# Performance work log

Measured on AMD Instinct MI355X. Metric: run time of the kernel, lower is better.

Reference implementation:

```python
import jax, jax.numpy as jnp
import numpy as np

D = 256      # wsi_projection_dim / SNN hidden
E = 1024     # wsi_embedding_dim
N = 60000    # num WSI patches
H = 8        # n_heads
DH = D // H  # head dim
K = 3        # int(6 * topk_ratio)
SIZES = (100, 200, 300, 400, 500, 600)
NC = 4       # num_classes
EPS = 1e-5


def _ln(x, g, b):
    m = x.mean(-1, keepdims=True)
    v = ((x - m) ** 2).mean(-1, keepdims=True)
    return (x - m) / jnp.sqrt(v + EPS) * g + b


def setup_inputs() -> dict:
    key = jax.random.key(0)
    ks = iter(jax.random.split(key, 64))
    sc = 0.02
    inp = {}
    inp["x_path"] = jax.random.normal(next(ks), (1, N, E), dtype=jnp.float32)
    for i, s in enumerate(SIZES):
        inp[f"x_omic{i+1}"] = jax.random.normal(next(ks), (s,), dtype=jnp.float32)
    # per-pathway SNN blocks: Linear(size,256)+ELU, Linear(256,256)+ELU
    for i, s in enumerate(SIZES):
        inp[f"sw1_{i}"] = sc * jax.random.normal(next(ks), (s, D), dtype=jnp.float32)
    inp["sb1"] = jnp.zeros((len(SIZES), D), jnp.float32)
    inp["sw2"] = sc * jax.random.normal(next(ks), (len(SIZES), D, D), dtype=jnp.float32)
    inp["sb2"] = jnp.zeros((len(SIZES), D), jnp.float32)
    # wsi projection
    inp["wp"] = sc * jax.random.normal(next(ks), (E, D), dtype=jnp.float32)
    inp["bp"] = jnp.zeros((D,), jnp.float32)
    # gene attention MLP 256->64->1
    inp["wa1"] = sc * jax.random.normal(next(ks), (D, 64), dtype=jnp.float32)
    inp["ba1"] = jnp.zeros((64,), jnp.float32)
    inp["wa2"] = sc * jax.random.normal(next(ks), (64, 1), dtype=jnp.float32)
    inp["ba2"] = jnp.zeros((1,), jnp.float32)
    # MultiheadAttention projections
    for nm in ("wq", "wk", "wv", "wo"):
        inp[nm] = sc * jax.random.normal(next(ks), (D, D), dtype=jnp.float32)
    for nm in ("bq", "bk", "bv", "bo"):
        inp[nm] = jnp.zeros((D,), jnp.float32)
    inp["ln1_g"] = jnp.ones((D,), jnp.float32)
    inp["ln1_b"] = jnp.zeros((D,), jnp.float32)
    # bilinear fusion 512->256->256
    inp["wf1"] = sc * jax.random.normal(next(ks), (2 * D, D), dtype=jnp.float32)
    inp["bf1"] = jnp.zeros((D,), jnp.float32)
    inp["wf2"] = sc * jax.random.normal(next(ks), (D, D), dtype=jnp.float32)
    inp["bf2"] = jnp.zeros((D,), jnp.float32)
    inp["ln2_g"] = jnp.ones((D,), jnp.float32)
    inp["ln2_b"] = jnp.zeros((D,), jnp.float32)
    inp["wc"] = sc * jax.random.normal(next(ks), (D, NC), dtype=jnp.float32)
    inp["bc"] = jnp.zeros((NC,), jnp.float32)
    return inp


def _forward(x_path, x_omics, sw1s, sb1, sw2, sb2, wp, bp, wa1, ba1, wa2, ba2,
             wq, bq, wk, bk, wv, bv, wo, bo, ln1_g, ln1_b,
             wf1, bf1, wf2, bf2, ln2_g, ln2_b, wc, bc):
    # per-pathway SNN (eval: AlphaDropout = identity)
    h = [jax.nn.elu(jax.nn.elu(x @ w1 + sb1[i]) @ sw2[i] + sb2[i])
         for i, (x, w1) in enumerate(zip(x_omics, sw1s))]
    bag = jnp.stack(h)[None]                      # [1, G, D]
    # gene selection: softmax -> topk -> gather (mask*gather == gather)
    scores = (jax.nn.relu(bag @ wa1 + ba1) @ wa2 + ba2)[..., 0]   # [1, G]
    attw = jax.nn.softmax(scores, axis=1)
    _, idx = jax.lax.top_k(attw, K)               # [1, K]
    selected = jnp.take_along_axis(bag, idx[..., None], axis=1)  # [1, K, D]
    # wsi projection (eval: Dropout = identity)
    wsi = jax.nn.relu(x_path @ wp + bp)           # [1, N, D]
    # cross-attention: queries = selected genes, keys/values = wsi patches
    q = (selected @ wq + bq).reshape(1, K, H, DH).transpose(0, 2, 1, 3)
    k_ = (wsi @ wk + bk).reshape(1, N, H, DH).transpose(0, 2, 1, 3)
    v_ = (wsi @ wv + bv).reshape(1, N, H, DH).transpose(0, 2, 1, 3)
    att = jax.nn.softmax(jnp.einsum('bhqd,bhkd->bhqk', q, k_) / np.float32(np.sqrt(DH)), axis=-1)
    attn_out = jnp.einsum('bhqk,bhkd->bhqd', att, v_).transpose(0, 2, 1, 3).reshape(1, K, D)
    attn_out = attn_out @ wo + bo                 # [1, K, D]
    # adaptive_avg_pool2d over N -> K bins (N divisible by K -> equal bins)
    pooled = wsi.reshape(1, K, N // K, D).mean(axis=2)  # [1, K, D]
    attended = _ln(attn_out + pooled, ln1_g, ln1_b)
    attended_mean = attended.mean(axis=1)         # [1, D]
    gene_features = selected.mean(axis=1)         # [1, D]
    comb = jnp.concatenate([attended_mean, gene_features], axis=1)  # [1, 2D]
    f = jax.nn.relu(comb @ wf1 + bf1)
    f = jax.nn.relu(f @ wf2 + bf2)
    fused = _ln(f + attended_mean, ln2_g, ln2_b)
    return fused @ wc + bc                        # [1, num_classes]


def reference(x_path, x_omic1, x_omic2, x_omic3, x_omic4, x_omic5, x_omic6,
              sw1_0, sw1_1, sw1_2, sw1_3, sw1_4, sw1_5, sb1, sw2, sb2,
              wp, bp, wa1, ba1, wa2, ba2,
              wq, bq, wk, bk, wv, bv, wo, bo, ln1_g, ln1_b,
              wf1, bf1, wf2, bf2, ln2_g, ln2_b, wc, bc):
    x_omics = (x_omic1, x_omic2, x_omic3, x_omic4, x_omic5, x_omic6)
    sw1s = (sw1_0, sw1_1, sw1_2, sw1_3, sw1_4, sw1_5)
    return _forward(x_path, x_omics, sw1s, sb1, sw2, sb2, wp, bp, wa1, ba1, wa2, ba2,
                    wq, bq, wk, bk, wv, bv, wo, bo, ln1_g, ln1_b,
                    wf1, bf1, wf2, bf2, ln2_g, ln2_b, wc, bc)
```

## Files before the change

### kernel.cpp

```cpp
#include <hip/hip_runtime.h>
#include <hip/hip_bf16.h>
#include <math.h>

typedef unsigned short ushort_t;
typedef __attribute__((ext_vector_type(8))) short bf16x8;
typedef __attribute__((ext_vector_type(4))) float f32x4;

#define NHQ 24
#define LN_EPS 1e-5f
#define NBLK_F 469
#define NBLK_A 938
#define NPOOL 256

#define WS_BAG 0
#define WS_SEL 1536
#define WS_GENE 2304
#define WS_PM 3584
#define WS_PL 28160
#define WS_PACC 52736
#define WS_PPOOL 839168
#define WS_ATTN 1232384
#define WS_POOLED 1233152
#define WS_BF16 1233920
#define U_WPT 0
#define U_WKT 262144
#define U_WVT 327680
#define U_QB  393216
#define U_WSIP 401408
#define WS_SPLIT_BYTES 36474880ULL

__device__ __forceinline__ ushort_t f2bf(float f) {
    __hip_bfloat16 h = __float2bfloat16(f);
    return *reinterpret_cast<ushort_t*>(&h);
}
__device__ __forceinline__ float bf2f(unsigned int u) {
    union { unsigned int i; float f; } c; c.i = u << 16; return c.f;
}
__device__ __forceinline__ unsigned int pk2(float a, float b) {
    return (unsigned int)f2bf(a) | ((unsigned int)f2bf(b) << 16);
}

__global__ void prep_kernel(const float* __restrict__ wp, const float* __restrict__ wk,
                            const float* __restrict__ wv, ushort_t* __restrict__ ub) {
    const int b = blockIdx.x, t = threadIdx.x;
    if (b < 16) {
        const int D16 = b;
        for (int i = 0; i < 64; ++i) {
            int f = t + i * 256;
            int K32 = f >> 9, r = f & 511;
            int lg = r >> 7, lm2 = (r >> 3) & 15, e = r & 7;
            int k = K32 * 32 + lg * 8 + e, d = D16 * 16 + lm2;
            ub[U_WPT + D16 * 16384 + f] = f2bf(wp[(size_t)k * 256 + d]);
        }
    } else if (b < 32) {
        const int D16 = b - 16;
        for (int i = 0; i < 16; ++i) {
            int f = t + i * 256;
            int K32 = f >> 9, r = f & 511;
            int lg = r >> 7, lm2 = (r >> 3) & 15, e = r & 7;
            int k = K32 * 32 + lg * 8 + e, d = D16 * 16 + lm2;
            ub[U_WKT + D16 * 4096 + f] = f2bf(wk[(size_t)k * 256 + d]);
        }
    } else {
        const int D16 = b - 32;
        for (int i = 0; i < 16; ++i) {
            int f = t + i * 256;
            int K32 = f >> 9, r = f & 511;
            int lg = r >> 7, lm2 = (r >> 3) & 15, e = r & 7;
            int k = K32 * 32 + lg * 8 + e, d = D16 * 16 + lm2;
            ub[U_WVT + D16 * 4096 + f] = f2bf(wv[(size_t)k * 256 + d]);
        }
    }
}

struct PrepArgs {
    const float* xo[6];
    const float* w1[6];
    int sz[6];
};

__global__ void snn_kernel(PrepArgs pa, const float* __restrict__ sb1,
                           const float* __restrict__ sw2, const float* __restrict__ sb2,
                           float* __restrict__ bag) {
    __shared__ float xsh[600];
    __shared__ float t1sh[256];
    const int i = blockIdx.x;
    const int t = threadIdx.x;
    const int s = pa.sz[i];
    const float* xo = pa.xo[i];
    const float* w1 = pa.w1[i];
    for (int j = t; j < s; j += 256) xsh[j] = xo[j];
    __syncthreads();
    float acc = sb1[i * 256 + t];
    for (int j = 0; j < s; ++j) acc += xsh[j] * w1[j * 256 + t];
    t1sh[t] = acc > 0.f ? acc : expm1f(acc);
    __syncthreads();
    float acc2 = sb2[i * 256 + t];
    const float* w2 = sw2 + (size_t)i * 256 * 256;
    for (int j = 0; j < 256; ++j) acc2 += t1sh[j] * w2[j * 256 + t];
    bag[i * 256 + t] = acc2 > 0.f ? acc2 : expm1f(acc2);
}

__global__ void select_kernel(const float* __restrict__ wa1, const float* __restrict__ ba1,
                              const float* __restrict__ wa2, const float* __restrict__ ba2,
                              const float* __restrict__ wq, const float* __restrict__ bq,
                              float* __restrict__ wsf, ushort_t* __restrict__ ub) {
    __shared__ float bsh[6][256];
    __shared__ float ysh[64];
    __shared__ float ssh[8];
    __shared__ int isel[3];
    const int t = threadIdx.x;
    for (int j = t; j < 1536; j += 256) ((float*)bsh)[j] = wsf[WS_BAG + j];
    __syncthreads();
    for (int i = 0; i < 6; ++i) {
        if (t < 64) {
            float acc = ba1[t];
            for (int j = 0; j < 256; ++j) acc += bsh[i][j] * wa1[j * 64 + t];
            ysh[t] = fmaxf(acc, 0.f) * wa2[t];
        }
        __syncthreads();
        if (t == 0) {
            float sc = ba2[0];
            for (int j = 0; j < 64; ++j) sc += ysh[j];
            ssh[i] = sc;
        }
        __syncthreads();
    }
    if (t == 0) {
        float sc[6];
        for (int i = 0; i < 6; ++i) sc[i] = ssh[i];
        for (int k = 0; k < 3; ++k) {
            int best = 0; float bv = sc[0];
            for (int i = 1; i < 6; ++i) if (sc[i] > bv) { bv = sc[i]; best = i; }
            isel[k] = best;
            sc[best] = -INFINITY;
        }
    }
    __syncthreads();
    float g = 0.f;
    for (int k = 0; k < 3; ++k) {
        float v = bsh[isel[k]][t];
        wsf[WS_SEL + k * 256 + t] = v;
        g += v;
    }
    wsf[WS_GENE + t] = g * (1.f / 3.f);
    for (int kq = 0; kq < 3; ++kq) {
        float acc = bq[t];
        const float* srow = bsh[isel[kq]];
        for (int j = 0; j < 256; ++j) acc += srow[j] * wq[j * 256 + t];
        float v = acc * 0.17677669529663687f;
        int hq = (t >> 5) * 3 + kq, dd = t & 31;
        ub[U_QB + hq * 32 + dd] = f2bf(v);
    }
}


#define PLOAD_X(xr, c) { \
    _Pragma("unroll") for (int i_ = 0; i_ < 4; ++i_) { \
        int f_ = tid + i_ * 512; int p_ = f_ >> 4, c4_ = f_ & 15; \
        if (n0 + p_ < 60000) \
            xr[i_] = *(const float4*)(xp + (size_t)(n0 + p_) * 1024 + (c) * 64 + c4_ * 4); \
        else { xr[i_].x = 0.f; xr[i_].y = 0.f; xr[i_].z = 0.f; xr[i_].w = 0.f; } } }

#define PSTORE_X(xr, buf) { \
    _Pragma("unroll") for (int i_ = 0; i_ < 4; ++i_) { \
        int f_ = tid + i_ * 512; int p_ = f_ >> 4, c4_ = f_ & 15; \
        int byte_ = (p_ * 128 + c4_ * 8) ^ ((p_ & 7) << 4); \
        uint2 u_; u_.x = pk2(xr[i_].x, xr[i_].y); u_.y = pk2(xr[i_].z, xr[i_].w); \
        *(uint2*)((buf) + byte_) = u_; } }

__global__ __launch_bounds__(512, 4) void proj_kernel(
    const float* __restrict__ xp, const float* __restrict__ bp,
    const ushort_t* __restrict__ ub, ushort_t* __restrict__ wsiP)
{
    __shared__ __align__(16) char xbuf[2][16384];
    const int tid = threadIdx.x;
    const int b = blockIdx.x;
    const int lane = tid & 63;
    const int w = tid >> 6;
    const int lm = lane & 15;
    const int lg = lane >> 4;
    const int wd0 = (w & 3) * 64;
    const int n0 = b * 128;
    const ushort_t* wpP = ub + U_WPT;

    f32x4 acc[16];
#pragma unroll
    for (int i = 0; i < 16; ++i) acc[i] = (f32x4){0.f, 0.f, 0.f, 0.f};

    float4 xr[4];
    PLOAD_X(xr, 0);
    PSTORE_X(xr, xbuf[0]);
    PLOAD_X(xr, 1);
    __syncthreads();
#pragma unroll 1
    for (int c = 0; c < 16; ++c) {
        const char* cur = xbuf[c & 1];
        if (c < 15) PSTORE_X(xr, xbuf[(c + 1) & 1]);
        if (c < 14) PLOAD_X(xr, c + 2);
#pragma unroll
        for (int ks = 0; ks < 2; ++ks) {
            bf16x8 wf[4];
#pragma unroll
            for (int dt = 0; dt < 4; ++dt)
                wf[dt] = *(const bf16x8*)(wpP + ((size_t)(((w & 3) * 4 + dt) * 32 + c * 2 + ks)) * 512 + lane * 8);
            bf16x8 bfr[4];
#pragma unroll
            for (int pt = 0; pt < 4; ++pt) {
                int p = (w >> 2) * 64 + pt * 16 + lm;
                int byte = (p * 128 + ks * 64 + lg * 16) ^ ((p & 7) << 4);
                bfr[pt] = *(const bf16x8*)(cur + byte);
            }
#pragma unroll
            for (int dt = 0; dt < 4; ++dt)
#pragma unroll
                for (int pt = 0; pt < 4; ++pt)
                    acc[dt * 4 + pt] = __builtin_amdgcn_mfma_f32_16x16x32_bf16(wf[dt], bfr[pt], acc[dt * 4 + pt], 0, 0, 0);
        }
        __syncthreads();
    }
#pragma unroll
    for (int dt = 0; dt < 4; ++dt) {
        int d0 = wd0 + dt * 16 + lg * 4;
        float4 bb = *(const float4*)(bp + d0);
        int ks2 = d0 >> 5, lg2 = (d0 >> 3) & 3, e0 = d0 & 7;
#pragma unroll
        for (int pt = 0; pt < 4; ++pt) {
            int p16 = b * 8 + (w >> 2) * 4 + pt;
            f32x4 v = acc[dt * 4 + pt];
            uint2 u;
            u.x = pk2(fmaxf(v[0] + bb.x, 0.f), fmaxf(v[1] + bb.y, 0.f));
            u.y = pk2(fmaxf(v[2] + bb.z, 0.f), fmaxf(v[3] + bb.w, 0.f));
            *(uint2*)(wsiP + (size_t)((p16 * 8 + ks2) * 4 + lg2) * 128 + lm * 8 + e0) = u;
        }
    }
}

__global__ __launch_bounds__(256, 4) void attn_kernel(
    const float* __restrict__ bk, const float* __restrict__ bv,
    const ushort_t* __restrict__ ub, const ushort_t* __restrict__ wsiP,
    float* __restrict__ wsf)
{
    __shared__ __align__(16) ushort_t kv_s[64 * 256];
    __shared__ __align__(16) ushort_t p_s[24 * 64];
    const int tid = threadIdx.x;
    const int b = blockIdx.x;
    const int lane = tid & 63, w = tid >> 6;
    const int lm = lane & 15, lg = lane >> 4;
    const int lmc = lm < 3 ? lm : 2;
    const int n0 = b * 64;
    const int wd0 = w * 64;
    const ushort_t* wkP = ub + U_WKT;
    const ushort_t* wvP = ub + U_WVT;

    {
        f32x4 acc[16];
#pragma unroll
        for (int i = 0; i < 16; ++i) acc[i] = (f32x4){0.f, 0.f, 0.f, 0.f};
#pragma unroll
        for (int ks = 0; ks < 8; ++ks) {
            bf16x8 wf[4], bfr[4];
#pragma unroll
            for (int dt = 0; dt < 4; ++dt)
                wf[dt] = *(const bf16x8*)(wkP + ((size_t)((w * 4 + dt) * 8 + ks)) * 512 + lane * 8);
#pragma unroll
            for (int pt = 0; pt < 4; ++pt)
                bfr[pt] = *(const bf16x8*)(wsiP + (size_t)(((b * 4 + pt) * 8 + ks) * 4 + lg) * 128 + lm * 8);
#pragma unroll
            for (int dt = 0; dt < 4; ++dt)
#pragma unroll
                for (int pt = 0; pt < 4; ++pt)
                    acc[dt * 4 + pt] = __builtin_amdgcn_mfma_f32_16x16x32_bf16(wf[dt], bfr[pt], acc[dt * 4 + pt], 0, 0, 0);
        }
#pragma unroll
        for (int dt = 0; dt < 4; ++dt) {
            int d0 = wd0 + dt * 16 + lg * 4;
            float4 bb = *(const float4*)(bk + d0);
#pragma unroll
            for (int pt = 0; pt < 4; ++pt) {
                int p = pt * 16 + lm;
                f32x4 v = acc[dt * 4 + pt];
                uint2 u;
                u.x = pk2(v[0] + bb.x, v[1] + bb.y);
                u.y = pk2(v[2] + bb.z, v[3] + bb.w);
                int byte = (p * 512 + d0 * 2) ^ ((p & 7) << 4);
                *(uint2*)((char*)kv_s + byte) = u;
            }
        }
    }
    __syncthreads();

    float m_reg[2], l_reg[2];
#pragma unroll
    for (int hh = 0; hh < 2; ++hh) {
        int h = w * 2 + hh;
        bf16x8 qf;
        if (lm < 3) qf = *(const bf16x8*)(ub + U_QB + (h * 3 + lm) * 32 + lg * 8);
        else { bf16x8 z = {0,0,0,0,0,0,0,0}; qf = z; }
        f32x4 sc[4];
#pragma unroll
        for (int blk = 0; blk < 4; ++blk) {
            sc[blk] = (f32x4){0.f, 0.f, 0.f, 0.f};
            int p = blk * 16 + lm;
            int byte = (p * 512 + (h * 32 + lg * 8) * 2) ^ ((p & 7) << 4);
            bf16x8 kf = *(const bf16x8*)((const char*)kv_s + byte);
            sc[blk] = __builtin_amdgcn_mfma_f32_16x16x32_bf16(kf, qf, sc[blk], 0, 0, 0);
        }
        float tmax = -INFINITY;
#pragma unroll
        for (int blk = 0; blk < 4; ++blk)
#pragma unroll
            for (int j = 0; j < 4; ++j) {
                int p = blk * 16 + lg * 4 + j;
                if (n0 + p >= 60000) sc[blk][j] = -INFINITY;
                tmax = fmaxf(tmax, sc[blk][j]);
            }
        tmax = fmaxf(tmax, __shfl_xor(tmax, 16));
        tmax = fmaxf(tmax, __shfl_xor(tmax, 32));
        float lsum = 0.f;
#pragma unroll
        for (int blk = 0; blk < 4; ++blk)
#pragma unroll
            for (int j = 0; j < 4; ++j) {
                float e = __expf(sc[blk][j] - tmax);
                sc[blk][j] = e;
                lsum += e;
            }
        lsum += __shfl_xor(lsum, 16);
        lsum += __shfl_xor(lsum, 32);
        m_reg[hh] = tmax;
        l_reg[hh] = lsum;
        if (lm < 3) {
#pragma unroll
            for (int blk = 0; blk < 4; ++blk) {
                int p0 = blk * 16 + lg * 4;
                *(unsigned int*)(p_s + (h * 3 + lm) * 64 + p0) = pk2(sc[blk][0], sc[blk][1]);
                *(unsigned int*)(p_s + (h * 3 + lm) * 64 + p0 + 2) = pk2(sc[blk][2], sc[blk][3]);
            }
        }
    }
    __syncthreads();

    {
        f32x4 acc[16];
#pragma unroll
        for (int i = 0; i < 16; ++i) acc[i] = (f32x4){0.f, 0.f, 0.f, 0.f};
#pragma unroll
        for (int ks = 0; ks < 8; ++ks) {
            bf16x8 wf[4], bfr[4];
#pragma unroll
            for (int dt = 0; dt < 4; ++dt)
                wf[dt] = *(const bf16x8*)(wvP + ((size_t)((w * 4 + dt) * 8 + ks)) * 512 + lane * 8);
#pragma unroll
            for (int pt = 0; pt < 4; ++pt)
                bfr[pt] = *(const bf16x8*)(wsiP + (size_t)(((b * 4 + pt) * 8 + ks) * 4 + lg) * 128 + lm * 8);
#pragma unroll
            for (int dt = 0; dt < 4; ++dt)
#pragma unroll
                for (int pt = 0; pt < 4; ++pt)
                    acc[dt * 4 + pt] = __builtin_amdgcn_mfma_f32_16x16x32_bf16(wf[dt], bfr[pt], acc[dt * 4 + pt], 0, 0, 0);
        }
        __syncthreads();
#pragma unroll
        for (int dt = 0; dt < 4; ++dt) {
            int d0 = wd0 + dt * 16 + lg * 4;
            float4 bb = *(const float4*)(bv + d0);
#pragma unroll
            for (int pt = 0; pt < 4; ++pt) {
                int p = pt * 16 + lm;
                f32x4 v = acc[dt * 4 + pt];
                float r[4] = {v[0] + bb.x, v[1] + bb.y, v[2] + bb.z, v[3] + bb.w};
#pragma unroll
                for (int j = 0; j < 4; ++j) {
                    int dd = d0 + j;
                    int byte = (dd * 128 + p * 2) ^ ((dd & 7) << 4);
                    *(ushort_t*)((char*)kv_s + byte) = f2bf(r[j]);
                }
            }
        }
    }
    __syncthreads();

    f32x4 pv[2][2];
#pragma unroll
    for (int hh = 0; hh < 2; ++hh)
#pragma unroll
        for (int nb = 0; nb < 2; ++nb) pv[hh][nb] = (f32x4){0.f, 0.f, 0.f, 0.f};
#pragma unroll
    for (int hh = 0; hh < 2; ++hh) {
        int h = w * 2 + hh;
#pragma unroll
        for (int ks = 0; ks < 2; ++ks) {
            bf16x8 pa = *(const bf16x8*)(p_s + (h * 3 + lmc) * 64 + ks * 32 + lg * 8);
#pragma unroll
            for (int nb = 0; nb < 2; ++nb) {
                int row = h * 32 + nb * 16 + lm;
                int byte = (row * 128 + (ks * 32 + lg * 8) * 2) ^ ((row & 7) << 4);
                bf16x8 vb = *(const bf16x8*)((const char*)kv_s + byte);
                pv[hh][nb] = __builtin_amdgcn_mfma_f32_16x16x32_bf16(pa, vb, pv[hh][nb], 0, 0, 0);
            }
        }
    }

    if (lg == 0) {
#pragma unroll
        for (int hh = 0; hh < 2; ++hh)
#pragma unroll
            for (int nb = 0; nb < 2; ++nb)
#pragma unroll
                for (int j = 0; j < 3; ++j) {
                    int hq = (w * 2 + hh) * 3 + j;
                    wsf[WS_PACC + b * 768 + hq * 32 + nb * 16 + lm] = pv[hh][nb][j];
                }
    }
    if (lm < 3 && lg == 0) {
#pragma unroll
        for (int hh = 0; hh < 2; ++hh) {
            int hq = (w * 2 + hh) * 3 + lm;
            wsf[WS_PM + b * 24 + hq] = m_reg[hh];
            wsf[WS_PL + b * 24 + hq] = l_reg[hh];
        }
    }
}

__global__ __launch_bounds__(256, 8) void pool_kernel(const ushort_t* __restrict__ wsiP,
                                                      float* __restrict__ wsf) {
    const int tid = threadIdx.x, b = blockIdx.x;
    const int lane = tid & 63;
    const int lm = lane & 15, lg = (lane >> 4) & 3;
    const int ks = ((b * 4) + (tid >> 6)) & 7;
    f32x4 s[3][2];
#pragma unroll
    for (int i = 0; i < 3; ++i) { s[i][0] = (f32x4){0,0,0,0}; s[i][1] = (f32x4){0,0,0,0}; }
    for (int sl = b * 256 + tid; sl < 1921024; sl += 65536) {
        int p16 = sl >> 9;
        if (p16 >= 3750) continue;
        uint4 u = *(const uint4*)(wsiP + (size_t)sl * 8);
        int bin = (p16 >= 2500) ? 2 : (p16 >= 1250 ? 1 : 0);
        f32x4 a, c;
        a[0] = bf2f(u.x & 0xffffu); a[1] = bf2f(u.x >> 16);
        a[2] = bf2f(u.y & 0xffffu); a[3] = bf2f(u.y >> 16);
        c[0] = bf2f(u.z & 0xffffu); c[1] = bf2f(u.z >> 16);
        c[2] = bf2f(u.w & 0xffffu); c[3] = bf2f(u.w >> 16);
        s[bin][0] += a; s[bin][1] += c;
    }
#pragma unroll
    for (int o = 1; o < 16; o <<= 1)
#pragma unroll
        for (int bin = 0; bin < 3; ++bin)
#pragma unroll
            for (int hv = 0; hv < 2; ++hv)
#pragma unroll
                for (int e = 0; e < 4; ++e)
                    s[bin][hv][e] += __shfl_xor(s[bin][hv][e], o);
    if (lm == 0) {
        int dbase = ks * 32 + lg * 8;
#pragma unroll
        for (int bin = 0; bin < 3; ++bin)
#pragma unroll
            for (int hv = 0; hv < 2; ++hv)
#pragma unroll
                for (int e = 0; e < 4; ++e)
                    wsf[WS_PPOOL + b * 768 + bin * 256 + dbase + hv * 4 + e] = s[bin][hv][e];
    } else if (lm == 1) {
        int dbase = (ks ^ 4) * 32 + lg * 8;
#pragma unroll
        for (int bin = 0; bin < 3; ++bin)
#pragma unroll
            for (int e = 0; e < 8; ++e)
                wsf[WS_PPOOL + b * 768 + bin * 256 + dbase + e] = 0.f;
    }
}

#define LOAD_X(xr, c) { \
    _Pragma("unroll") for (int i_ = 0; i_ < 4; ++i_) { \
        int f_ = tid + i_ * 512; int p_ = f_ >> 4, c4_ = f_ & 15; \
        if (n0 + p_ < 60000) \
            xr[i_] = *(const float4*)(xp + (size_t)(n0 + p_) * 1024 + (c) * 64 + c4_ * 4); \
        else { xr[i_].x = 0.f; xr[i_].y = 0.f; xr[i_].z = 0.f; xr[i_].w = 0.f; } } }

#define STORE_X(xr) { \
    _Pragma("unroll") for (int i_ = 0; i_ < 4; ++i_) { \
        int f_ = tid + i_ * 512; int p_ = f_ >> 4, c4_ = f_ & 15; \
        int byte_ = (p_ * 128 + c4_ * 8) ^ ((p_ & 7) << 4); \
        uint2 u_; u_.x = pk2(xr[i_].x, xr[i_].y); u_.y = pk2(xr[i_].z, xr[i_].w); \
        *(uint2*)((char*)x_s + byte_) = u_; } }

#define LOAD_W1(dst, c) { \
    _Pragma("unroll") for (int ks_ = 0; ks_ < 2; ++ks_) \
    _Pragma("unroll") for (int dt_ = 0; dt_ < 4; ++dt_) \
        dst[ks_ * 4 + dt_] = *(const bf16x8*)(wpP + ((size_t)(((w & 3) * 4 + dt_) * 32 + (c) * 2 + ks_)) * 512 + lane * 8); }

#define MFMA_CHUNK(wf) { \
    _Pragma("unroll") for (int ks_ = 0; ks_ < 2; ++ks_) { \
        bf16x8 bfr_[4]; \
        _Pragma("unroll") for (int pt_ = 0; pt_ < 4; ++pt_) { \
            int p_ = wp0 + pt_ * 16 + lm; \
            int byte_ = (p_ * 128 + ks_ * 64 + lg * 16) ^ ((p_ & 7) << 4); \
            bfr_[pt_] = *(const bf16x8*)((const char*)x_s + byte_); } \
        _Pragma("unroll") for (int dt_ = 0; dt_ < 4; ++dt_) \
        _Pragma("unroll") for (int pt_ = 0; pt_ < 4; ++pt_) \
            acc[dt_ * 4 + pt_] = __builtin_amdgcn_mfma_f32_16x16x32_bf16(wf[ks_ * 4 + dt_], bfr_[pt_], acc[dt_ * 4 + pt_], 0, 0, 0); } }

__global__ __launch_bounds__(512, 2) void main_kernel(
    const float* __restrict__ xp, const float* __restrict__ bp,
    const float* __restrict__ bk, const float* __restrict__ bv,
    const ushort_t* __restrict__ ub, float* __restrict__ wsf)
{
    __shared__ __align__(16) ushort_t wsi_s[128 * 256];
    __shared__ __align__(16) ushort_t kv_s[128 * 256];
    __shared__ __align__(16) ushort_t x_s[128 * 64];
    __shared__ __align__(16) ushort_t p_s[NHQ * 128];
    __shared__ float mlc_s[72];

    const int tid = threadIdx.x;
    const int b = blockIdx.x;
    const int lane = tid & 63;
    const int w = tid >> 6;
    const int lm = lane & 15;
    const int lg = lane >> 4;
    const int lmc = (lm < 3) ? lm : 2;
    const int wd0 = (w & 3) * 64;
    const int wp0 = (w >> 2) * 64;

    const ushort_t* wpP = ub + U_WPT;
    const ushort_t* wkP = ub + U_WKT;
    const ushort_t* wvP = ub + U_WVT;

    bf16x8 qfrag;
    if (lm < 3) qfrag = *(const bf16x8*)(ub + U_QB + (w * 3 + lm) * 32 + lg * 8);
    else { bf16x8 z = {0,0,0,0,0,0,0,0}; qfrag = z; }

    if (tid < 24) { mlc_s[tid] = -INFINITY; mlc_s[24 + tid] = 0.f; mlc_s[48 + tid] = 0.f; }

    f32x4 pv[2] = {{0.f,0.f,0.f,0.f},{0.f,0.f,0.f,0.f}};
    float pl0 = 0.f, pl1 = 0.f, pl2 = 0.f;
    __syncthreads();

    const int n0 = b * 128;
    {
        f32x4 acc[16];
#pragma unroll
        for (int i = 0; i < 16; ++i) acc[i] = (f32x4){0.f,0.f,0.f,0.f};
        float4 xr[4];
        bf16x8 wA[8], wB[8];
        LOAD_X(xr, 0); LOAD_W1(wA, 0);
        for (int c = 0; c < 16; c += 2) {
            __syncthreads();
            STORE_X(xr);
            __syncthreads();
            LOAD_X(xr, c + 1); LOAD_W1(wB, c + 1);
            MFMA_CHUNK(wA);
            __syncthreads();
            STORE_X(xr);
            __syncthreads();
            if (c + 2 < 16) { LOAD_X(xr, c + 2); LOAD_W1(wA, c + 2); }
            MFMA_CHUNK(wB);
        }
#pragma unroll
        for (int dt = 0; dt < 4; ++dt) {
            int d0 = wd0 + dt * 16 + lg * 4;
            float4 bb = *(const float4*)(bp + d0);
#pragma unroll
            for (int pt = 0; pt < 4; ++pt) {
                int p = wp0 + pt * 16 + lm;
                f32x4 v = acc[dt * 4 + pt];
                uint2 u;
                u.x = pk2(fmaxf(v[0] + bb.x, 0.f), fmaxf(v[1] + bb.y, 0.f));
                u.y = pk2(fmaxf(v[2] + bb.z, 0.f), fmaxf(v[3] + bb.w, 0.f));
                int byte = (p * 512 + d0 * 2) ^ ((p & 7) << 4);
                *(uint2*)((char*)wsi_s + byte) = u;
            }
        }
    }
    __syncthreads();

    {
        int d = tid & 255, half = tid >> 8;
#pragma unroll 16
        for (int pp = 0; pp < 64; ++pp) {
            int p = half * 64 + pp;
            int gp = n0 + p;
            int byte = (p * 512 + d * 2) ^ ((p & 7) << 4);
            float v = bf2f((unsigned int)*(const ushort_t*)((const char*)wsi_s + byte));
            pl0 += (gp < 20000) ? v : 0.f;
            pl1 += (gp >= 20000 && gp < 40000) ? v : 0.f;
            pl2 += (gp >= 40000 && gp < 60000) ? v : 0.f;
        }
    }

    {
        f32x4 acc2[16];
#pragma unroll
        for (int i = 0; i < 16; ++i) acc2[i] = (f32x4){0.f,0.f,0.f,0.f};
#pragma unroll
        for (int ks = 0; ks < 8; ++ks) {
            bf16x8 wf[4];
#pragma unroll
            for (int dt = 0; dt < 4; ++dt)
                wf[dt] = *(const bf16x8*)(wkP + ((size_t)(((w & 3) * 4 + dt) * 8 + ks)) * 512 + lane * 8);
            bf16x8 bfr[4];
#pragma unroll
            for (int pt = 0; pt < 4; ++pt) {
                int p = wp0 + pt * 16 + lm;
                int byte = (p * 512 + (ks * 32 + lg * 8) * 2) ^ ((p & 7) << 4);
                bfr[pt] = *(const bf16x8*)((const char*)wsi_s + byte);
            }
#pragma unroll
            for (int dt = 0; dt < 4; ++dt)
#pragma unroll
                for (int pt = 0; pt < 4; ++pt)
                    acc2[dt * 4 + pt] = __builtin_amdgcn_mfma_f32_16x16x32_bf16(wf[dt], bfr[pt], acc2[dt * 4 + pt], 0, 0, 0);
        }
#pragma unroll
        for (int dt = 0; dt < 4; ++dt) {
            int d0 = wd0 + dt * 16 + lg * 4;
            float4 bb = *(const float4*)(bk + d0);
#pragma unroll
            for (int pt = 0; pt < 4; ++pt) {
                int p = wp0 + pt * 16 + lm;
                f32x4 v = acc2[dt * 4 + pt];
                uint2 u;
                u.x = pk2(v[0] + bb.x, v[1] + bb.y);
                u.y = pk2(v[2] + bb.z, v[3] + bb.w);
                int byte = (p * 512 + d0 * 2) ^ ((p & 7) << 4);
                *(uint2*)((char*)kv_s + byte) = u;
            }
        }
    }
    __syncthreads();

    {
        f32x4 sc[8];
#pragma unroll
        for (int blk = 0; blk < 8; ++blk) {
            sc[blk] = (f32x4){0.f,0.f,0.f,0.f};
            int p = blk * 16 + lm;
            int byte = (p * 512 + (w * 32 + lg * 8) * 2) ^ ((p & 7) << 4);
            bf16x8 kf = *(const bf16x8*)((const char*)kv_s + byte);
            sc[blk] = __builtin_amdgcn_mfma_f32_16x16x32_bf16(kf, qfrag, sc[blk], 0, 0, 0);
        }
        float m_old = mlc_s[w * 3 + lmc];
        float tmax = -INFINITY;
#pragma unroll
        for (int blk = 0; blk < 8; ++blk)
#pragma unroll
            for (int j = 0; j < 4; ++j) {
                int p = blk * 16 + lg * 4 + j;
                if (n0 + p >= 60000) sc[blk][j] = -INFINITY;
                tmax = fmaxf(tmax, sc[blk][j]);
            }
        tmax = fmaxf(tmax, __shfl_xor(tmax, 16));
        tmax = fmaxf(tmax, __shfl_xor(tmax, 32));
        float mnew = fmaxf(m_old, tmax);
        float lsum = 0.f;
#pragma unroll
        for (int blk = 0; blk < 8; ++blk)
#pragma unroll
            for (int j = 0; j < 4; ++j) {
                float e = __expf(sc[blk][j] - mnew);
                sc[blk][j] = e;
                lsum += e;
            }
        lsum += __shfl_xor(lsum, 16);
        lsum += __shfl_xor(lsum, 32);
        float corr = __expf(m_old - mnew);
        if (lane < 3) {
            mlc_s[w * 3 + lane] = mnew;
            mlc_s[24 + w * 3 + lane] = mlc_s[24 + w * 3 + lane] * corr + lsum;
            mlc_s[48 + w * 3 + lane] = corr;
        }
        if (lm < 3) {
#pragma unroll
            for (int blk = 0; blk < 8; ++blk) {
                int p0 = blk * 16 + lg * 4;
                *(unsigned int*)(p_s + (w * 3 + lm) * 128 + p0) = pk2(sc[blk][0], sc[blk][1]);
                *(unsigned int*)(p_s + (w * 3 + lm) * 128 + p0 + 2) = pk2(sc[blk][2], sc[blk][3]);
            }
        }
    }
    __syncthreads();

    {
        f32x4 acc2[16];
#pragma unroll
        for (int i = 0; i < 16; ++i) acc2[i] = (f32x4){0.f,0.f,0.f,0.f};
#pragma unroll
        for (int ks = 0; ks < 8; ++ks) {
            bf16x8 wf[4];
#pragma unroll
            for (int dt = 0; dt < 4; ++dt)
                wf[dt] = *(const bf16x8*)(wvP + ((size_t)(((w & 3) * 4 + dt) * 8 + ks)) * 512 + lane * 8);
            bf16x8 bfr[4];
#pragma unroll
            for (int pt = 0; pt < 4; ++pt) {
                int p = wp0 + pt * 16 + lm;
                int byte = (p * 512 + (ks * 32 + lg * 8) * 2) ^ ((p & 7) << 4);
                bfr[pt] = *(const bf16x8*)((const char*)wsi_s + byte);
            }
#pragma unroll
            for (int dt = 0; dt < 4; ++dt)
#pragma unroll
                for (int pt = 0; pt < 4; ++pt)
                    acc2[dt * 4 + pt] = __builtin_amdgcn_mfma_f32_16x16x32_bf16(wf[dt], bfr[pt], acc2[dt * 4 + pt], 0, 0, 0);
        }
#pragma unroll
        for (int dt = 0; dt < 4; ++dt) {
            int d0 = wd0 + dt * 16 + lg * 4;
            float4 bb = *(const float4*)(bv + d0);
#pragma unroll
            for (int pt = 0; pt < 4; ++pt) {
                int p = wp0 + pt * 16 + lm;
                f32x4 v = acc2[dt * 4 + pt];
                float r[4] = {v[0] + bb.x, v[1] + bb.y, v[2] + bb.z, v[3] + bb.w};
#pragma unroll
                for (int j = 0; j < 4; ++j) {
                    int dd = d0 + j;
                    int byte = (dd * 256 + p * 2) ^ ((dd & 14) << 2);
                    *(ushort_t*)((char*)kv_s + byte) = f2bf(r[j]);
                }
            }
        }
    }
    __syncthreads();

    {
        float cj[4];
#pragma unroll
        for (int j = 0; j < 4; ++j) {
            int q = lg * 4 + j;
            cj[j] = mlc_s[48 + w * 3 + (q < 3 ? q : 2)];
        }
#pragma unroll
        for (int nb = 0; nb < 2; ++nb)
#pragma unroll
            for (int j = 0; j < 4; ++j) pv[nb][j] *= cj[j];
#pragma unroll
        for (int ks = 0; ks < 4; ++ks) {
            bf16x8 pa = *(const bf16x8*)(p_s + (w * 3 + lmc) * 128 + ks * 32 + lg * 8);
#pragma unroll
            for (int nb = 0; nb < 2; ++nb) {
                int row = w * 32 + nb * 16 + lm;
                int byte = (row * 256 + (ks * 32 + lg * 8) * 2) ^ ((row & 14) << 2);
                bf16x8 vb = *(const bf16x8*)((const char*)kv_s + byte);
                pv[nb] = __builtin_amdgcn_mfma_f32_16x16x32_bf16(pa, vb, pv[nb], 0, 0, 0);
            }
        }
    }

    __syncthreads();
    {
        float* scr = (float*)x_s;
        int d = tid & 255, half = tid >> 8;
        scr[half * 768 + 0 * 256 + d] = pl0;
        scr[half * 768 + 1 * 256 + d] = pl1;
        scr[half * 768 + 2 * 256 + d] = pl2;
    }
    __syncthreads();
    if (tid < 256) {
        float* scr = (float*)x_s;
#pragma unroll
        for (int bin = 0; bin < 3; ++bin)
            wsf[WS_PPOOL + b * 768 + bin * 256 + tid] = scr[bin * 256 + tid] + scr[768 + bin * 256 + tid];
    }
    if (tid < 24) {
        wsf[WS_PM + b * 24 + tid] = mlc_s[tid];
        wsf[WS_PL + b * 24 + tid] = mlc_s[24 + tid];
    }
    if (lg == 0) {
#pragma unroll
        for (int nb = 0; nb < 2; ++nb)
#pragma unroll
            for (int j = 0; j < 3; ++j) {
                int hq = w * 3 + j, dd = nb * 16 + lm;
                wsf[WS_PACC + b * 768 + hq * 32 + dd] = pv[nb][j];
            }
    }
}

__global__ __launch_bounds__(256) void combine_kernel(float* __restrict__ wsf, int nblk, int npool) {
    const int bidx = blockIdx.x;
    const int t = threadIdx.x;
    if (bidx < NHQ) {
        const int hq = bidx;
        __shared__ float w_s[1024];
        __shared__ float mred[4];
        __shared__ float lred[4];
        __shared__ float ored[8][32];
        float m = -INFINITY;
        for (int b = t; b < nblk; b += 256) m = fmaxf(m, wsf[WS_PM + b * 24 + hq]);
#pragma unroll
        for (int o = 32; o > 0; o >>= 1) m = fmaxf(m, __shfl_xor(m, o));
        if ((t & 63) == 0) mred[t >> 6] = m;
        __syncthreads();
        const float M = fmaxf(fmaxf(mred[0], mred[1]), fmaxf(mred[2], mred[3]));
        float L = 0.f;
        for (int b = t; b < nblk; b += 256) {
            float wv = __expf(wsf[WS_PM + b * 24 + hq] - M);
            w_s[b] = wv;
            L += wv * wsf[WS_PL + b * 24 + hq];
        }
#pragma unroll
        for (int o = 32; o > 0; o >>= 1) L += __shfl_xor(L, o);
        if ((t & 63) == 0) lred[t >> 6] = L;
        __syncthreads();
        const float Lt = lred[0] + lred[1] + lred[2] + lred[3];
        const int g = t >> 5, dd = t & 31;
        float O = 0.f;
        for (int b = g; b < nblk; b += 8)
            O += wsf[WS_PACC + b * 768 + hq * 32 + dd] * w_s[b];
        ored[g][dd] = O;
        __syncthreads();
        if (t < 32) {
            float s = 0.f;
#pragma unroll
            for (int g2 = 0; g2 < 8; ++g2) s += ored[g2][t];
            int h = hq / 3, kq = hq - h * 3;
            wsf[WS_ATTN + kq * 256 + h * 32 + t] = s / Lt;
        }
    } else {
        const int bin = bidx - NHQ;
        const int d = t;
        float s0 = 0.f, s1 = 0.f, s2 = 0.f, s3 = 0.f;
        int b = 0;
        for (; b + 3 < npool; b += 4) {
            s0 += wsf[WS_PPOOL + (b + 0) * 768 + bin * 256 + d];
            s1 += wsf[WS_PPOOL + (b + 1) * 768 + bin * 256 + d];
            s2 += wsf[WS_PPOOL + (b + 2) * 768 + bin * 256 + d];
            s3 += wsf[WS_PPOOL + (b + 3) * 768 + bin * 256 + d];
        }
        for (; b < npool; ++b) s0 += wsf[WS_PPOOL + b * 768 + bin * 256 + d];
        wsf[WS_POOLED + bin * 256 + d] = (s0 + s1 + s2 + s3) * (1.f / 20000.f);
    }
}

__device__ __forceinline__ float block_sum256(float v, float* red, int t) {
#pragma unroll
    for (int o = 32; o > 0; o >>= 1) v += __shfl_xor(v, o);
    if ((t & 63) == 0) red[t >> 6] = v;
    __syncthreads();
    float r = red[0] + red[1] + red[2] + red[3];
    __syncthreads();
    return r;
}

__global__ void final_kernel(const float* __restrict__ wo, const float* __restrict__ bo,
                             const float* __restrict__ ln1g, const float* __restrict__ ln1b,
                             const float* __restrict__ wf1, const float* __restrict__ bf1,
                             const float* __restrict__ wf2, const float* __restrict__ bf2,
                             const float* __restrict__ ln2g, const float* __restrict__ ln2b,
                             const float* __restrict__ wc, const float* __restrict__ bc,
                             float* __restrict__ wsf, float* __restrict__ out) {
    __shared__ float attnC[3][256];
    __shared__ float att[3][256];
    __shared__ float amean[256];
    __shared__ float gf[256];
    __shared__ float f1[256];
    __shared__ float red[256];
    const int t = threadIdx.x;
    for (int j = t; j < 768; j += 256) ((float*)attnC)[j] = wsf[WS_ATTN + j];
    gf[t] = wsf[WS_GENE + t];
    __syncthreads();
    for (int kq = 0; kq < 3; ++kq) {
        float acc = bo[t];
        for (int j = 0; j < 256; ++j) acc += attnC[kq][j] * wo[j * 256 + t];
        float x = acc + wsf[WS_POOLED + kq * 256 + t];
        float m = block_sum256(x, red, t) * (1.f / 256.f);
        float dv = x - m;
        float var = block_sum256(dv * dv, red, t) * (1.f / 256.f);
        att[kq][t] = dv * rsqrtf(var + LN_EPS) * ln1g[t] + ln1b[t];
    }
    __syncthreads();
    amean[t] = (att[0][t] + att[1][t] + att[2][t]) * (1.f / 3.f);
    __syncthreads();
    {
        float acc = bf1[t];
        for (int j = 0; j < 256; ++j) acc += amean[j] * wf1[j * 256 + t];
        for (int j = 0; j < 256; ++j) acc += gf[j] * wf1[(256 + j) * 256 + t];
        f1[t] = fmaxf(acc, 0.f);
    }
    __syncthreads();
    float acc2 = bf2[t];
    for (int j = 0; j < 256; ++j) acc2 += f1[j] * wf2[j * 256 + t];
    float y = fmaxf(acc2, 0.f) + amean[t];
    float m2 = block_sum256(y, red, t) * (1.f / 256.f);
    float dv2 = y - m2;
    float v2 = block_sum256(dv2 * dv2, red, t) * (1.f / 256.f);
    float fused = dv2 * rsqrtf(v2 + LN_EPS) * ln2g[t] + ln2b[t];
    red[t] = fused;
    __syncthreads();
    if (t < 4) {
        float o = bc[t];
        for (int j = 0; j < 256; ++j) o += red[j] * wc[j * 4 + t];
        out[t] = o;
    }
}

extern "C" void kernel_launch(void* const* d_in, const int* in_sizes, int n_in,
                              void* d_out, int out_size, void* d_ws, size_t ws_size,
                              hipStream_t stream) {
    const float* xp = (const float*)d_in[0];
    PrepArgs pa;
    for (int i = 0; i < 6; ++i) {
        pa.xo[i] = (const float*)d_in[1 + i];
        pa.w1[i] = (const float*)d_in[7 + i];
        pa.sz[i] = in_sizes[1 + i];
    }
    const float* sb1 = (const float*)d_in[13];
    const float* sw2 = (const float*)d_in[14];
    const float* sb2 = (const float*)d_in[15];
    const float* wp  = (const float*)d_in[16];
    const float* bp  = (const float*)d_in[17];
    const float* wa1 = (const float*)d_in[18];
    const float* ba1 = (const float*)d_in[19];
    const float* wa2 = (const float*)d_in[20];
    const float* ba2 = (const float*)d_in[21];
    const float* wq  = (const float*)d_in[22];
    const float* wk  = (const float*)d_in[23];
    const float* wv  = (const float*)d_in[24];
    const float* wo  = (const float*)d_in[25];
    const float* bq  = (const float*)d_in[26];
    const float* bk  = (const float*)d_in[27];
    const float* bv  = (const float*)d_in[28];
    const float* bo  = (const float*)d_in[29];
    const float* ln1g = (const float*)d_in[30];
    const float* ln1b = (const float*)d_in[31];
    const float* wf1 = (const float*)d_in[32];
    const float* bf1 = (const float*)d_in[33];
    const float* wf2 = (const float*)d_in[34];
    const float* bf2 = (const float*)d_in[35];
    const float* ln2g = (const float*)d_in[36];
    const float* ln2b = (const float*)d_in[37];
    const float* wc  = (const float*)d_in[38];
    const float* bc  = (const float*)d_in[39];

    float* wsf = (float*)d_ws;
    float* out = (float*)d_out;
    ushort_t* ub = (ushort_t*)(wsf + WS_BF16);

    prep_kernel<<<dim3(48), dim3(256), 0, stream>>>(wp, wk, wv, ub);
    snn_kernel<<<dim3(6), dim3(256), 0, stream>>>(pa, sb1, sw2, sb2, wsf + WS_BAG);
    select_kernel<<<dim3(1), dim3(256), 0, stream>>>(wa1, ba1, wa2, ba2, wq, bq, wsf, ub);

    if (ws_size >= WS_SPLIT_BYTES) {
        ushort_t* wsiP = ub + U_WSIP;
        proj_kernel<<<dim3(NBLK_F), dim3(512), 0, stream>>>(xp, bp, ub, wsiP);
        attn_kernel<<<dim3(NBLK_A), dim3(256), 0, stream>>>(bk, bv, ub, wsiP, wsf);
        pool_kernel<<<dim3(NPOOL), dim3(256), 0, stream>>>(wsiP, wsf);
        combine_kernel<<<dim3(27), dim3(256), 0, stream>>>(wsf, NBLK_A, NPOOL);
    } else {
        main_kernel<<<dim3(NBLK_F), dim3(512), 0, stream>>>(xp, bp, bk, bv, ub, wsf);
        combine_kernel<<<dim3(27), dim3(256), 0, stream>>>(wsf, NBLK_F, NBLK_F);
    }
    final_kernel<<<dim3(1), dim3(256), 0, stream>>>(wo, bo, ln1g, ln1b, wf1, bf1, wf2, bf2,
                                                    ln2g, ln2b, wc, bc, wsf, out);
}
```

Measured before the change: 761.0 us.

## Fuse mean-pooling into attention kernel and halve projection block size

The separate pool kernel is removed. Each attention block now also sums its own 64 patches of projected features into per-bin partial pools, which removes one launch and one extra full pass over the projected buffer. The projection kernel moves to 256-thread blocks covering 64 patches each, giving 938 blocks that line up with the attention grid and raise block count. In exchange the combine step has more pool partials to reduce, and the workspace grows to hold them.

```diff
diff --git a/kernel.cpp b/kernel.cpp
--- a/kernel.cpp
+++ b/kernel.cpp
@@ -9,8 +9,7 @@
 #define NHQ 24
 #define LN_EPS 1e-5f
 #define NBLK_F 469
-#define NBLK_A 938
-#define NPOOL 256
+#define NBLK_P 938
 
 #define WS_BAG 0
 #define WS_SEL 1536
@@ -19,15 +18,15 @@
 #define WS_PL 28160
 #define WS_PACC 52736
 #define WS_PPOOL 839168
-#define WS_ATTN 1232384
-#define WS_POOLED 1233152
-#define WS_BF16 1233920
+#define WS_ATTN 1625600
+#define WS_POOLED 1626368
+#define WS_BF16 1627136
 #define U_WPT 0
 #define U_WKT 262144
 #define U_WVT 327680
 #define U_QB  393216
 #define U_WSIP 401408
-#define WS_SPLIT_BYTES 36474880ULL
+#define WS_SPLIT_BYTES 38047744ULL
 
 __device__ __forceinline__ ushort_t f2bf(float f) {
     __hip_bfloat16 h = __float2bfloat16(f);
@@ -155,33 +154,32 @@
 }
 
 
-#define PLOAD_X(xr, c) { \
+#define P2LOAD_X(xr, c) { \
     _Pragma("unroll") for (int i_ = 0; i_ < 4; ++i_) { \
-        int f_ = tid + i_ * 512; int p_ = f_ >> 4, c4_ = f_ & 15; \
+        int f_ = tid + i_ * 256; int p_ = f_ >> 4, c4_ = f_ & 15; \
         if (n0 + p_ < 60000) \
             xr[i_] = *(const float4*)(xp + (size_t)(n0 + p_) * 1024 + (c) * 64 + c4_ * 4); \
         else { xr[i_].x = 0.f; xr[i_].y = 0.f; xr[i_].z = 0.f; xr[i_].w = 0.f; } } }
 
-#define PSTORE_X(xr, buf) { \
+#define P2STORE_X(xr, buf) { \
     _Pragma("unroll") for (int i_ = 0; i_ < 4; ++i_) { \
-        int f_ = tid + i_ * 512; int p_ = f_ >> 4, c4_ = f_ & 15; \
+        int f_ = tid + i_ * 256; int p_ = f_ >> 4, c4_ = f_ & 15; \
         int byte_ = (p_ * 128 + c4_ * 8) ^ ((p_ & 7) << 4); \
         uint2 u_; u_.x = pk2(xr[i_].x, xr[i_].y); u_.y = pk2(xr[i_].z, xr[i_].w); \
         *(uint2*)((buf) + byte_) = u_; } }
 
-__global__ __launch_bounds__(512, 4) void proj_kernel(
+__global__ __launch_bounds__(256, 4) void proj_kernel(
     const float* __restrict__ xp, const float* __restrict__ bp,
     const ushort_t* __restrict__ ub, ushort_t* __restrict__ wsiP)
 {
-    __shared__ __align__(16) char xbuf[2][16384];
+    __shared__ __align__(16) char xbuf[2][8192];
     const int tid = threadIdx.x;
     const int b = blockIdx.x;
     const int lane = tid & 63;
     const int w = tid >> 6;
     const int lm = lane & 15;
     const int lg = lane >> 4;
-    const int wd0 = (w & 3) * 64;
-    const int n0 = b * 128;
+    const int n0 = b * 64;
     const ushort_t* wpP = ub + U_WPT;
 
     f32x4 acc[16];
@@ -189,25 +187,25 @@
     for (int i = 0; i < 16; ++i) acc[i] = (f32x4){0.f, 0.f, 0.f, 0.f};
 
     float4 xr[4];
-    PLOAD_X(xr, 0);
-    PSTORE_X(xr, xbuf[0]);
-    PLOAD_X(xr, 1);
+    P2LOAD_X(xr, 0);
+    P2STORE_X(xr, xbuf[0]);
+    P2LOAD_X(xr, 1);
     __syncthreads();
 #pragma unroll 1
     for (int c = 0; c < 16; ++c) {
         const char* cur = xbuf[c & 1];
-        if (c < 15) PSTORE_X(xr, xbuf[(c + 1) & 1]);
-        if (c < 14) PLOAD_X(xr, c + 2);
+        if (c < 15) P2STORE_X(xr, xbuf[(c + 1) & 1]);
+        if (c < 14) P2LOAD_X(xr, c + 2);
 #pragma unroll
         for (int ks = 0; ks < 2; ++ks) {
             bf16x8 wf[4];
 #pragma unroll
             for (int dt = 0; dt < 4; ++dt)
-                wf[dt] = *(const bf16x8*)(wpP + ((size_t)(((w & 3) * 4 + dt) * 32 + c * 2 + ks)) * 512 + lane * 8);
+                wf[dt] = *(const bf16x8*)(wpP + ((size_t)((w * 4 + dt) * 32 + c * 2 + ks)) * 512 + lane * 8);
             bf16x8 bfr[4];
 #pragma unroll
             for (int pt = 0; pt < 4; ++pt) {
-                int p = (w >> 2) * 64 + pt * 16 + lm;
+                int p = pt * 16 + lm;
                 int byte = (p * 128 + ks * 64 + lg * 16) ^ ((p & 7) << 4);
                 bfr[pt] = *(const bf16x8*)(cur + byte);
             }
@@ -221,12 +219,12 @@
     }
 #pragma unroll
     for (int dt = 0; dt < 4; ++dt) {
-        int d0 = wd0 + dt * 16 + lg * 4;
+        int d0 = w * 64 + dt * 16 + lg * 4;
         float4 bb = *(const float4*)(bp + d0);
         int ks2 = d0 >> 5, lg2 = (d0 >> 3) & 3, e0 = d0 & 7;
 #pragma unroll
         for (int pt = 0; pt < 4; ++pt) {
-            int p16 = b * 8 + (w >> 2) * 4 + pt;
+            int p16 = b * 4 + pt;
             f32x4 v = acc[dt * 4 + pt];
             uint2 u;
             u.x = pk2(fmaxf(v[0] + bb.x, 0.f), fmaxf(v[1] + bb.y, 0.f));
@@ -421,54 +419,52 @@
             wsf[WS_PL + b * 24 + hq] = l_reg[hh];
         }
     }
-}
-
-__global__ __launch_bounds__(256, 8) void pool_kernel(const ushort_t* __restrict__ wsiP,
-                                                      float* __restrict__ wsf) {
-    const int tid = threadIdx.x, b = blockIdx.x;
-    const int lane = tid & 63;
-    const int lm = lane & 15, lg = (lane >> 4) & 3;
-    const int ks = ((b * 4) + (tid >> 6)) & 7;
-    f32x4 s[3][2];
-#pragma unroll
-    for (int i = 0; i < 3; ++i) { s[i][0] = (f32x4){0,0,0,0}; s[i][1] = (f32x4){0,0,0,0}; }
-    for (int sl = b * 256 + tid; sl < 1921024; sl += 65536) {
-        int p16 = sl >> 9;
-        if (p16 >= 3750) continue;
-        uint4 u = *(const uint4*)(wsiP + (size_t)sl * 8);
-        int bin = (p16 >= 2500) ? 2 : (p16 >= 1250 ? 1 : 0);
-        f32x4 a, c;
-        a[0] = bf2f(u.x & 0xffffu); a[1] = bf2f(u.x >> 16);
-        a[2] = bf2f(u.y & 0xffffu); a[3] = bf2f(u.y >> 16);
-        c[0] = bf2f(u.z & 0xffffu); c[1] = bf2f(u.z >> 16);
-        c[2] = bf2f(u.w & 0xffffu); c[3] = bf2f(u.w >> 16);
-        s[bin][0] += a; s[bin][1] += c;
-    }
-#pragma unroll
-    for (int o = 1; o < 16; o <<= 1)
-#pragma unroll
-        for (int bin = 0; bin < 3; ++bin)
-#pragma unroll
-            for (int hv = 0; hv < 2; ++hv)
-#pragma unroll
-                for (int e = 0; e < 4; ++e)
-                    s[bin][hv][e] += __shfl_xor(s[bin][hv][e], o);
-    if (lm == 0) {
-        int dbase = ks * 32 + lg * 8;
-#pragma unroll
-        for (int bin = 0; bin < 3; ++bin)
-#pragma unroll
-            for (int hv = 0; hv < 2; ++hv)
-#pragma unroll
-                for (int e = 0; e < 4; ++e)
-                    wsf[WS_PPOOL + b * 768 + bin * 256 + dbase + hv * 4 + e] = s[bin][hv][e];
-    } else if (lm == 1) {
-        int dbase = (ks ^ 4) * 32 + lg * 8;
-#pragma unroll
-        for (int bin = 0; bin < 3; ++bin)
-#pragma unroll
-            for (int e = 0; e < 8; ++e)
-                wsf[WS_PPOOL + b * 768 + bin * 256 + dbase + e] = 0.f;
+
+#pragma unroll 1
+    for (int it = 0; it < 2; ++it) {
+        float pl0[8], pl1[8], pl2[8];
+#pragma unroll
+        for (int e = 0; e < 8; ++e) { pl0[e] = 0.f; pl1[e] = 0.f; pl2[e] = 0.f; }
+        int slot = tid + it * 256;
+        int ks = slot >> 6, lg2 = (slot >> 4) & 3, lm2 = slot & 15;
+#pragma unroll
+        for (int pt = 0; pt < 4; ++pt) {
+            int p16 = b * 4 + pt;
+            if (p16 < 3750) {
+                uint4 u = *(const uint4*)(wsiP + (size_t)((p16 * 8 + ks) * 4 + lg2) * 128 + lm2 * 8);
+                float v0 = bf2f(u.x & 0xffffu), v1 = bf2f(u.x >> 16);
+                float v2 = bf2f(u.y & 0xffffu), v3 = bf2f(u.y >> 16);
+                float v4 = bf2f(u.z & 0xffffu), v5 = bf2f(u.z >> 16);
+                float v6 = bf2f(u.w & 0xffffu), v7 = bf2f(u.w >> 16);
+                if (p16 >= 2500) {
+                    pl2[0]+=v0; pl2[1]+=v1; pl2[2]+=v2; pl2[3]+=v3;
+                    pl2[4]+=v4; pl2[5]+=v5; pl2[6]+=v6; pl2[7]+=v7;
+                } else if (p16 >= 1250) {
+                    pl1[0]+=v0; pl1[1]+=v1; pl1[2]+=v2; pl1[3]+=v3;
+                    pl1[4]+=v4; pl1[5]+=v5; pl1[6]+=v6; pl1[7]+=v7;
+                } else {
+                    pl0[0]+=v0; pl0[1]+=v1; pl0[2]+=v2; pl0[3]+=v3;
+                    pl0[4]+=v4; pl0[5]+=v5; pl0[6]+=v6; pl0[7]+=v7;
+                }
+            }
+        }
+#pragma unroll
+        for (int o = 1; o < 16; o <<= 1)
+#pragma unroll
+            for (int e = 0; e < 8; ++e) {
+                pl0[e] += __shfl_xor(pl0[e], o);
+                pl1[e] += __shfl_xor(pl1[e], o);
+                pl2[e] += __shfl_xor(pl2[e], o);
+            }
+        if (lm2 == 0) {
+            int dbase = ks * 32 + lg2 * 8;
+#pragma unroll
+            for (int e = 0; e < 8; ++e) {
+                wsf[WS_PPOOL + b * 768 + 0 * 256 + dbase + e] = pl0[e];
+                wsf[WS_PPOOL + b * 768 + 1 * 256 + dbase + e] = pl1[e];
+                wsf[WS_PPOOL + b * 768 + 2 * 256 + dbase + e] = pl2[e];
+            }
+        }
     }
 }
 
@@ -944,10 +940,9 @@
 
     if (ws_size >= WS_SPLIT_BYTES) {
         ushort_t* wsiP = ub + U_WSIP;
-        proj_kernel<<<dim3(NBLK_F), dim3(512), 0, stream>>>(xp, bp, ub, wsiP);
-        attn_kernel<<<dim3(NBLK_A), dim3(256), 0, stream>>>(bk, bv, ub, wsiP, wsf);
-        pool_kernel<<<dim3(NPOOL), dim3(256), 0, stream>>>(wsiP, wsf);
-        combine_kernel<<<dim3(27), dim3(256), 0, stream>>>(wsf, NBLK_A, NPOOL);
+        proj_kernel<<<dim3(NBLK_P), dim3(256), 0, stream>>>(xp, bp, ub, wsiP);
+        attn_kernel<<<dim3(NBLK_P), dim3(256), 0, stream>>>(bk, bv, ub, wsiP, wsf);
+        combine_kernel<<<dim3(27), dim3(256), 0, stream>>>(wsf, NBLK_P, NBLK_P);
     } else {
         main_kernel<<<dim3(NBLK_F), dim3(512), 0, stream>>>(xp, bp, bk, bv, ub, wsf);
         combine_kernel<<<dim3(27), dim3(256), 0, stream>>>(wsf, NBLK_F, NBLK_F);
```

Result: no change. 770.8 us (+1.3%).
